# Kernel optimization log

Hardware: AMD Instinct MI355X
Metric: run time of the kernel (lower is better)

The kernel has to match this reference:

```python
import jax, jax.numpy as jnp
import numpy as np

LATENT = 32
GRID = 32
G1 = GRID + 1  # 33 samples per axis (align_corners grid)
HID = 128
N_POINTS = 1048576


def _trilinear_sample(emb, points):
    """Faithful F.grid_sample(mode='bilinear', padding_mode='zeros', align_corners=True).
    emb: [(G1)^3, C] flat table; points: [n,3] in [-1,1], (x,y,z) -> (W,H,D)."""
    C = emb.shape[1]
    # torch .view(1, C, D, H, W) on the flat [(G1)^3 * C] buffer: same reshape here.
    vol = emb.reshape(C, G1, G1, G1).transpose(1, 2, 3, 0)  # [D, H, W, C]
    # align_corners=True: u in [-1,1] -> pixel coord (u+1)/2 * (size-1)
    coords = (points + 1.0) * (0.5 * (G1 - 1))
    x, y, z = coords[:, 0], coords[:, 1], coords[:, 2]
    x0 = jnp.floor(x); y0 = jnp.floor(y); z0 = jnp.floor(z)
    fx = x - x0; fy = y - y0; fz = z - z0
    x0i = x0.astype(jnp.int32); y0i = y0.astype(jnp.int32); z0i = z0.astype(jnp.int32)
    x1i = x0i + 1; y1i = y0i + 1; z1i = z0i + 1

    def corner(zi, yi, xi, w):
        valid = ((zi >= 0) & (zi < G1) & (yi >= 0) & (yi < G1)
                 & (xi >= 0) & (xi < G1))
        zc = jnp.clip(zi, 0, G1 - 1)
        yc = jnp.clip(yi, 0, G1 - 1)
        xc = jnp.clip(xi, 0, G1 - 1)
        v = vol[zc, yc, xc]  # [n, C] gather
        return v * (w * valid.astype(w.dtype))[:, None]

    wx0, wx1 = 1.0 - fx, fx
    wy0, wy1 = 1.0 - fy, fy
    wz0, wz1 = 1.0 - fz, fz
    lat = (corner(z0i, y0i, x0i, wz0 * wy0 * wx0)
           + corner(z0i, y0i, x1i, wz0 * wy0 * wx1)
           + corner(z0i, y1i, x0i, wz0 * wy1 * wx0)
           + corner(z0i, y1i, x1i, wz0 * wy1 * wx1)
           + corner(z1i, y0i, x0i, wz1 * wy0 * wx0)
           + corner(z1i, y0i, x1i, wz1 * wy0 * wx1)
           + corner(z1i, y1i, x0i, wz1 * wy1 * wx0)
           + corner(z1i, y1i, x1i, wz1 * wy1 * wx1))
    return lat  # [n, C]


def setup_inputs() -> dict:
    key = jax.random.key(0)
    ks = jax.random.split(key, 8)
    points = jax.random.uniform(ks[0], (N_POINTS, 3), dtype=jnp.float32)  # in [0,1) subset of [-1,1]
    emb = jax.random.normal(ks[1], (G1 ** 3, LATENT), dtype=jnp.float32)
    w1 = jax.random.normal(ks[2], (LATENT, HID), dtype=jnp.float32) * 0.05
    b1 = jax.random.normal(ks[3], (HID,), dtype=jnp.float32) * 0.05
    w2 = jax.random.normal(ks[4], (HID, HID), dtype=jnp.float32) * 0.05
    b2 = jax.random.normal(ks[5], (HID,), dtype=jnp.float32) * 0.05
    w3 = jax.random.normal(ks[6], (HID, 1), dtype=jnp.float32) * 0.05
    b3 = jax.random.normal(ks[7], (1,), dtype=jnp.float32) * 0.05
    return {"points": points, "emb": emb, "w1": w1, "b1": b1,
            "w2": w2, "b2": b2, "w3": w3, "b3": b3}


def reference(points, emb, w1, b1, w2, b2, w3, b3):
    lat = _trilinear_sample(emb, points)                # [n, latent]
    h = jax.nn.relu(lat @ w1 + b1)                      # [n, hid]
    h = jax.nn.relu(h @ w2 + b2)                        # [n, hid]
    sdf = jnp.tanh(h @ w3 + b3)                         # [n, 1]
    return sdf
```

## Files before the change

kernel.cpp:

```cpp
#include <hip/hip_runtime.h>
#include <hip/hip_bf16.h>

#define NPTS 1048576
#define G1I  33
#define NV   35937
#define NC   32
#define HIDD 128

typedef _Float16 h8  __attribute__((ext_vector_type(8)));
typedef _Float16 h4  __attribute__((ext_vector_type(4)));
typedef __fp16   p2  __attribute__((ext_vector_type(2)));
typedef float    f4  __attribute__((ext_vector_type(4)));

#define AS_GLOBAL(p) ((const __attribute__((address_space(1))) char*)(p))
#define AS_LDS(p)    ((__attribute__((address_space(3))) char*)(p))

#define WS_A1  0
#define WS_A2  8192
#define WS_EMB 65536
#define WS_NEED (WS_EMB + NV*NC*2)


__global__ __launch_bounds__(256) void vox_prep(
    const float* __restrict__ emb, const float* __restrict__ w1,
    const float* __restrict__ w2, char* __restrict__ ws)
{
    __shared__ _Float16 tile[256][NC];
    const int b = blockIdx.x, t = threadIdx.x;
    _Float16* embh = (_Float16*)(ws + WS_EMB);
    if (b < 141) {
        const int v = b*256 + t;
        #pragma unroll
        for (int c = 0; c < NC; ++c) {
            float val = (v < NV) ? emb[c*NV + v] : 0.f;
            tile[t][c] = (_Float16)val;
        }
        __syncthreads();
        if (v < NV) {
            uint4* dst = (uint4*)(embh + v*NC);
            const uint4* src = (const uint4*)&tile[t][0];
            #pragma unroll
            for (int j = 0; j < 4; ++j) dst[j] = src[j];
        }
    } else if (b < 149) {
        const int t2 = b - 141;
        const int ks = t >> 6, l = t & 63;
        const int gq = l >> 4, colh = l & 15;
        _Float16* a2f = (_Float16*)(ws + WS_A2);
        h8 fr;
        #pragma unroll
        for (int i = 0; i < 8; ++i) {
            const int k = 32*ks + 16*(i>>2) + 4*gq + (i&3);
            fr[i] = (_Float16)w2[k*HIDD + 16*t2 + colh];
        }
        *(h8*)(a2f + ((t2*4+ks)*64 + l)*8) = fr;
    } else {
        _Float16* a1f = (_Float16*)(ws + WS_A1);
        #pragma unroll
        for (int it = 0; it < 2; ++it) {
            const int item = t + it*256;
            const int t8 = item >> 6, l = item & 63;
            const int gq = l >> 4, colh = l & 15;
            h8 fr;
            #pragma unroll
            for (int i = 0; i < 8; ++i) {
                const int k = 16*(i>>2) + 4*gq + (i&3);
                fr[i] = (_Float16)w1[k*HIDD + 16*t8 + colh];
            }
            *(h8*)(a1f + (t8*64 + l)*8) = fr;
        }
    }
}

union SmemU {
    _Float16 latl[256][40];
    uint4    a2l[2048];
};

__global__ __launch_bounds__(256, 4) void vox_main(
    const float* __restrict__ points, const char* __restrict__ ws,
    const float* __restrict__ b1, const float* __restrict__ b2,
    const float* __restrict__ w3, const float* __restrict__ b3v,
    float* __restrict__ out)
{
    __shared__ SmemU sm;

    const int tid  = threadIdx.x;
    const int lane = tid & 63;
    const int wv   = tid >> 6;
    const int gq   = lane >> 4;
    const int colh = lane & 15;

    const _Float16* embh = (const _Float16*)(ws + WS_EMB);
    const int p = blockIdx.x*256 + tid;
    const float px = points[3*p+0], py = points[3*p+1], pz = points[3*p+2];
    const float xc = (px + 1.f)*16.f, yc = (py + 1.f)*16.f, zc = (pz + 1.f)*16.f;
    const float xf = floorf(xc), yf = floorf(yc), zf = floorf(zc);
    const float fx = xc - xf, fy = yc - yf, fz = zc - zf;
    const int x0 = (int)xf, y0 = (int)yf, z0 = (int)zf;
    const float wzv[2] = {1.f-fz, fz}, wyv[2] = {1.f-fy, fy}, wxv[2] = {1.f-fx, fx};

    h8 acc8[4];
    #pragma unroll
    for (int j = 0; j < 4; ++j) acc8[j] = (h8){0,0,0,0,0,0,0,0};
    #pragma unroll
    for (int cz = 0; cz < 2; ++cz)
    #pragma unroll
    for (int cy = 0; cy < 2; ++cy) {
        const int vb = ((z0+cz)*G1I + (y0+cy))*G1I + x0;
        const float wzy = wzv[cz]*wyv[cy];
        #pragma unroll
        for (int cx = 0; cx < 2; ++cx) {
            const _Float16 wh = (_Float16)(wzy * wxv[cx]);
            const h8 wp = {wh,wh,wh,wh,wh,wh,wh,wh};
            const h8* rowp = (const h8*)(embh + (vb + cx)*NC);
            #pragma unroll
            for (int j = 0; j < 4; ++j) acc8[j] += wp * rowp[j];
        }
    }

    {
        uint4* lr = (uint4*)&sm.latl[tid][0];
        #pragma unroll
        for (int j = 0; j < 4; ++j) lr[j] = *(uint4*)&acc8[j];
    }
    asm volatile("s_waitcnt lgkmcnt(0)" ::: "memory");

    const h8* a1g = (const h8*)(ws + WS_A1);
    h8 a1fr[8];
    #pragma unroll
    for (int t8 = 0; t8 < 8; ++t8) a1fr[t8] = a1g[t8*64 + lane];

    h8 B2f[4][4];
    #pragma unroll
    for (int pt = 0; pt < 4; ++pt) {
        const int row = wv*64 + pt*16 + colh;
        const h4 blo = *(const h4*)&sm.latl[row][4*gq];
        const h4 bhi = *(const h4*)&sm.latl[row][16 + 4*gq];
        h8 bf;
        #pragma unroll
        for (int j = 0; j < 4; ++j) { bf[j] = blo[j]; bf[4+j] = bhi[j]; }
        f4 acc1[8];
        #pragma unroll
        for (int t8 = 0; t8 < 8; ++t8) acc1[t8] = *(const f4*)(b1 + 16*t8 + 4*gq);
        #pragma unroll
        for (int t8 = 0; t8 < 8; ++t8)
            acc1[t8] = __builtin_amdgcn_mfma_f32_16x16x32_f16(a1fr[t8], bf, acc1[t8], 0, 0, 0);
        #pragma unroll
        for (int ks = 0; ks < 4; ++ks) {
            union { h8 v; p2 h[4]; } u;
            const p2 z = {(__fp16)0, (__fp16)0};
            u.h[0] = __builtin_elementwise_max(__builtin_amdgcn_cvt_pkrtz(acc1[2*ks  ][0], acc1[2*ks  ][1]), z);
            u.h[1] = __builtin_elementwise_max(__builtin_amdgcn_cvt_pkrtz(acc1[2*ks  ][2], acc1[2*ks  ][3]), z);
            u.h[2] = __builtin_elementwise_max(__builtin_amdgcn_cvt_pkrtz(acc1[2*ks+1][0], acc1[2*ks+1][1]), z);
            u.h[3] = __builtin_elementwise_max(__builtin_amdgcn_cvt_pkrtz(acc1[2*ks+1][2], acc1[2*ks+1][3]), z);
            B2f[pt][ks] = u.v;
        }
    }

    __syncthreads();
    {
        const uint4* a2g = (const uint4*)(ws + WS_A2);
        #pragma unroll
        for (int j = 0; j < 8; ++j) {
            const uint4* gsrc = a2g + (j*256 + wv*64 + lane);
            uint4*       ldst = ((uint4*)sm.a2l) + (j*256 + wv*64);
            __builtin_amdgcn_global_load_lds(
                (const __attribute__((address_space(1))) void*)AS_GLOBAL(gsrc),
                (__attribute__((address_space(3))) void*)AS_LDS(ldst),
                16, 0, 0);
        }
    }
    asm volatile("s_waitcnt vmcnt(0)" ::: "memory");
    __syncthreads();

    float part[4] = {0.f, 0.f, 0.f, 0.f};
    #pragma unroll
    for (int t2 = 0; t2 < 8; ++t2) {
        const f4 b2q = *(const f4*)(b2 + 16*t2 + 4*gq);
        const f4 w3q = *(const f4*)(w3 + 16*t2 + 4*gq);
        f4 acc2[4];
        #pragma unroll
        for (int pt = 0; pt < 4; ++pt) acc2[pt] = b2q;
        #pragma unroll
        for (int ks = 0; ks < 4; ++ks) {
            const h8 a2fr = *(const h8*)&sm.a2l[(t2*4 + ks)*64 + lane];
            #pragma unroll
            for (int pt = 0; pt < 4; ++pt)
                acc2[pt] = __builtin_amdgcn_mfma_f32_16x16x32_f16(a2fr, B2f[pt][ks], acc2[pt], 0, 0, 0);
        }
        #pragma unroll
        for (int pt = 0; pt < 4; ++pt)
            #pragma unroll
            for (int r = 0; r < 4; ++r)
                part[pt] += fmaxf(acc2[pt][r], 0.f) * w3q[r];
    }

    float sv = 0.f;
    #pragma unroll
    for (int pt = 0; pt < 4; ++pt) {
        float s = part[pt];
        s += __shfl_xor(s, 16);
        s += __shfl_xor(s, 32);
        if (gq == pt) sv = s;
    }
    const float zi = sv + b3v[0];
    const float e  = __expf(2.f*zi);
    out[blockIdx.x*256 + tid] = (e - 1.f) / (e + 1.f);
}

extern "C" void kernel_launch(void* const* d_in, const int* in_sizes, int n_in,
                              void* d_out, int out_size, void* d_ws, size_t ws_size,
                              hipStream_t stream)
{
    const float* points = (const float*)d_in[0];
    const float* emb    = (const float*)d_in[1];
    const float* w1     = (const float*)d_in[2];
    const float* b1     = (const float*)d_in[3];
    const float* w2     = (const float*)d_in[4];
    const float* b2     = (const float*)d_in[5];
    const float* w3     = (const float*)d_in[6];
    const float* b3     = (const float*)d_in[7];
    float* out = (float*)d_out;
    char*  ws  = (char*)d_ws;
    if (ws_size < (size_t)WS_NEED) return;

    hipLaunchKernelGGL(vox_prep, dim3(150), dim3(256), 0, stream, emb, w1, w2, ws);
    hipLaunchKernelGGL(vox_main, dim3(NPTS/256), dim3(256), 0, stream,
                       points, ws, b1, b2, w3, b3, out);
}
```

Baseline: 162.5 us.

## Cooperative channel-split embedding gather and early async W2 LDS load

```diff
diff --git a/kernel.cpp b/kernel.cpp
--- a/kernel.cpp
+++ b/kernel.cpp
@@ -72,24 +72,33 @@
     }
 }
 
-union SmemU {
-    _Float16 latl[256][40];
-    uint4    a2l[2048];
-};
-
-__global__ __launch_bounds__(256, 4) void vox_main(
+__global__ __launch_bounds__(256) void vox_main(
     const float* __restrict__ points, const char* __restrict__ ws,
     const float* __restrict__ b1, const float* __restrict__ b2,
     const float* __restrict__ w3, const float* __restrict__ b3v,
     float* __restrict__ out)
 {
-    __shared__ SmemU sm;
+    __shared__ _Float16 latl[256][40];
+    __shared__ uint4    a2l[2048];
 
     const int tid  = threadIdx.x;
     const int lane = tid & 63;
     const int wv   = tid >> 6;
     const int gq   = lane >> 4;
     const int colh = lane & 15;
+
+    {
+        const uint4* a2g = (const uint4*)(ws + WS_A2);
+        #pragma unroll
+        for (int j = 0; j < 8; ++j) {
+            const uint4* gsrc = a2g + (j*256 + wv*64 + lane);
+            uint4*       ldst = ((uint4*)a2l) + (j*256 + wv*64);
+            __builtin_amdgcn_global_load_lds(
+                (const __attribute__((address_space(1))) void*)AS_GLOBAL(gsrc),
+                (__attribute__((address_space(3))) void*)AS_LDS(ldst),
+                16, 0, 0);
+        }
+    }
 
     const _Float16* embh = (const _Float16*)(ws + WS_EMB);
     const int p = blockIdx.x*256 + tid;
@@ -97,33 +106,40 @@
     const float xc = (px + 1.f)*16.f, yc = (py + 1.f)*16.f, zc = (pz + 1.f)*16.f;
     const float xf = floorf(xc), yf = floorf(yc), zf = floorf(zc);
     const float fx = xc - xf, fy = yc - yf, fz = zc - zf;
-    const int x0 = (int)xf, y0 = (int)yf, z0 = (int)zf;
-    const float wzv[2] = {1.f-fz, fz}, wyv[2] = {1.f-fy, fy}, wxv[2] = {1.f-fx, fx};
-
-    h8 acc8[4];
-    #pragma unroll
-    for (int j = 0; j < 4; ++j) acc8[j] = (h8){0,0,0,0,0,0,0,0};
-    #pragma unroll
-    for (int cz = 0; cz < 2; ++cz)
-    #pragma unroll
-    for (int cy = 0; cy < 2; ++cy) {
-        const int vb = ((z0+cz)*G1I + (y0+cy))*G1I + x0;
-        const float wzy = wzv[cz]*wyv[cy];
-        #pragma unroll
-        for (int cx = 0; cx < 2; ++cx) {
-            const _Float16 wh = (_Float16)(wzy * wxv[cx]);
+    const int vb = (((int)zf)*G1I + (int)yf)*G1I + (int)xf;
+
+    const int q  = lane >> 2;
+    const int ch = lane & 3;
+    h8 accch[4];
+    #pragma unroll
+    for (int sh = 0; sh < 4; ++sh) {
+        const int s = sh*16 + q;
+        const float fxs = __shfl(fx, s);
+        const float fys = __shfl(fy, s);
+        const float fzs = __shfl(fz, s);
+        const int   vbs = __shfl(vb, s);
+        const float wx1 = fxs, wx0 = 1.f - fxs;
+        const float wy1 = fys, wy0 = 1.f - fys;
+        const float wz1 = fzs, wz0 = 1.f - fzs;
+        float w8c[8];
+        w8c[0] = wz0*wy0*wx0; w8c[1] = wz0*wy0*wx1;
+        w8c[2] = wz0*wy1*wx0; w8c[3] = wz0*wy1*wx1;
+        w8c[4] = wz1*wy0*wx0; w8c[5] = wz1*wy0*wx1;
+        w8c[6] = wz1*wy1*wx0; w8c[7] = wz1*wy1*wx1;
+        h8 a = (h8){0,0,0,0,0,0,0,0};
+        #pragma unroll
+        for (int c = 0; c < 8; ++c) {
+            const int off = (c>>2)*(G1I*G1I) + ((c>>1)&1)*G1I + (c&1);
+            const h8 v = *(const h8*)(embh + (vbs + off)*NC + ch*8);
+            const _Float16 wh = (_Float16)w8c[c];
             const h8 wp = {wh,wh,wh,wh,wh,wh,wh,wh};
-            const h8* rowp = (const h8*)(embh + (vb + cx)*NC);
-            #pragma unroll
-            for (int j = 0; j < 4; ++j) acc8[j] += wp * rowp[j];
-        }
-    }
-
-    {
-        uint4* lr = (uint4*)&sm.latl[tid][0];
-        #pragma unroll
-        for (int j = 0; j < 4; ++j) lr[j] = *(uint4*)&acc8[j];
-    }
+            a += wp * v;
+        }
+        accch[sh] = a;
+    }
+    #pragma unroll
+    for (int sh = 0; sh < 4; ++sh)
+        *(uint4*)&latl[wv*64 + sh*16 + q][8*ch] = *(uint4*)&accch[sh];
     asm volatile("s_waitcnt lgkmcnt(0)" ::: "memory");
 
     const h8* a1g = (const h8*)(ws + WS_A1);
@@ -135,8 +151,8 @@
     #pragma unroll
     for (int pt = 0; pt < 4; ++pt) {
         const int row = wv*64 + pt*16 + colh;
-        const h4 blo = *(const h4*)&sm.latl[row][4*gq];
-        const h4 bhi = *(const h4*)&sm.latl[row][16 + 4*gq];
+        const h4 blo = *(const h4*)&latl[row][4*gq];
+        const h4 bhi = *(const h4*)&latl[row][16 + 4*gq];
         h8 bf;
         #pragma unroll
         for (int j = 0; j < 4; ++j) { bf[j] = blo[j]; bf[4+j] = bhi[j]; }
@@ -158,19 +174,6 @@
         }
     }
 
-    __syncthreads();
-    {
-        const uint4* a2g = (const uint4*)(ws + WS_A2);
-        #pragma unroll
-        for (int j = 0; j < 8; ++j) {
-            const uint4* gsrc = a2g + (j*256 + wv*64 + lane);
-            uint4*       ldst = ((uint4*)sm.a2l) + (j*256 + wv*64);
-            __builtin_amdgcn_global_load_lds(
-                (const __attribute__((address_space(1))) void*)AS_GLOBAL(gsrc),
-                (__attribute__((address_space(3))) void*)AS_LDS(ldst),
-                16, 0, 0);
-        }
-    }
     asm volatile("s_waitcnt vmcnt(0)" ::: "memory");
     __syncthreads();
 
@@ -184,7 +187,7 @@
         for (int pt = 0; pt < 4; ++pt) acc2[pt] = b2q;
         #pragma unroll
         for (int ks = 0; ks < 4; ++ks) {
-            const h8 a2fr = *(const h8*)&sm.a2l[(t2*4 + ks)*64 + lane];
+            const h8 a2fr = *(const h8*)&a2l[(t2*4 + ks)*64 + lane];
             #pragma unroll
             for (int pt = 0; pt < 4; ++pt)
                 acc2[pt] = __builtin_amdgcn_mfma_f32_16x16x32_f16(a2fr, B2f[pt][ks], acc2[pt], 0, 0, 0);
```

New measurement: 141.7 us. 1.15x faster.
